# Performance work log

Measured on AMD Instinct MI355X. Metric: run time of the kernel, lower is better.

Reference implementation:

```python
import jax, jax.numpy as jnp
import numpy as np

B, S, D = 4, 4096, 1024
DFF = 4 * D
ACTIVE = 1024  # ceil(S * 0.25)


def setup_inputs() -> dict:
    key = jax.random.key(0)
    ks = jax.random.split(key, 4)
    x = jax.random.normal(ks[0], (B, S, D), dtype=jnp.float32)
    rw = jax.random.normal(ks[1], (D,), dtype=jnp.float32) * 0.02
    rb = jnp.zeros((1,), dtype=jnp.float32)
    w1 = jax.random.normal(ks[2], (D, DFF), dtype=jnp.float32) * 0.02
    b1 = jnp.zeros((DFF,), dtype=jnp.float32)
    w2 = jax.random.normal(ks[3], (DFF, D), dtype=jnp.float32) * 0.02
    b2 = jnp.zeros((D,), dtype=jnp.float32)
    return {"x": x, "rw": rw, "rb": rb, "w1": w1, "b1": b1,
            "w2": w2, "b2": b2, "active_tokens": ACTIVE}


def reference(x, rw, rb, w1, b1, w2, b2, active_tokens):
    b, s, d = x.shape
    # router: Linear(n_embd, 1) -> [B, S] scores
    scores = jnp.einsum('bsd,d->bs', x, rw) + rb[0]
    # top-k tokens per batch row
    _, idx = jax.lax.top_k(scores, active_tokens)          # [B, K] int32
    sel = jnp.take_along_axis(x, idx[..., None], axis=1)   # [B, K, D]
    # dense MLP on selected tokens (exact GELU as in torch nn.GELU)
    h = jax.nn.gelu(jnp.einsum('bkd,df->bkf', sel, w1) + b1, approximate=False)
    out = jnp.einsum('bkf,fd->bkd', h, w2) + b2            # [B, K, D]
    # sigmoid gate from router scores of selected tokens
    gates = jax.nn.sigmoid(jnp.take_along_axis(scores, idx, axis=1))  # [B, K]
    out = out * gates[..., None]
    # scatter back into zeros at selected positions
    flat_idx = (idx + jnp.arange(b, dtype=idx.dtype)[:, None] * s).reshape(-1)
    flat_out = jnp.zeros((b * s, d), dtype=out.dtype)
    flat_out = flat_out.at[flat_idx].set(out.reshape(-1, d))
    return flat_out.reshape(b, s, d)
```

## Files before the change

### kernel.cpp

```cpp
#include <hip/hip_runtime.h>
#include <hip/hip_bf16.h>
#include <cstdint>
#include <cstddef>

#define Bz 4
#define Sz 4096
#define Dz 1024
#define DFFz 4096
#define KACT 1024

typedef __bf16 bf16;
typedef __attribute__((ext_vector_type(8))) __bf16 bf16x8;
typedef __attribute__((ext_vector_type(4))) __bf16 bf16x4;
typedef __attribute__((ext_vector_type(4))) float f32x4;

__device__ __forceinline__ void async16(const void* g, void* l) {
  __builtin_amdgcn_global_load_lds(
      (const __attribute__((address_space(1))) void*)g,
      (__attribute__((address_space(3))) void*)l, 16, 0, 0);
}

__global__ __launch_bounds__(256) void prep_k(const float* __restrict__ x,
                                              const float* __restrict__ rw,
                                              const float* __restrict__ rb,
                                              float* __restrict__ scores,
                                              float4* __restrict__ out4,
                                              const float* __restrict__ w1,
                                              bf16* __restrict__ w1T,
                                              const float* __restrict__ w2,
                                              bf16* __restrict__ w2T) {
  __shared__ float t[32][33];
  const int bid = blockIdx.x;
  const int tid = threadIdx.x;
  if (bid < 4096) {
    int row = bid * 4 + (tid >> 6);
    int lane = tid & 63;
    const float4* xr = (const float4*)(x + (size_t)row * Dz);
    const float4* wr = (const float4*)rw;
    float acc = 0.f;
#pragma unroll
    for (int i = 0; i < 4; ++i) {
      float4 a = xr[lane + i * 64];
      float4 w = wr[lane + i * 64];
      acc += a.x * w.x + a.y * w.y + a.z * w.z + a.w * w.w;
    }
#pragma unroll
    for (int d = 32; d; d >>= 1) acc += __shfl_down(acc, d, 64);
    if (lane == 0) scores[row] = acc + rb[0];
    float4* o = out4 + (size_t)bid * 4 * (Dz / 4);
    const float4 z = make_float4(0.f, 0.f, 0.f, 0.f);
#pragma unroll
    for (int i = 0; i < 4; ++i) o[tid + i * 256] = z;
  } else {
    const float* in; bf16* outp; int R, C, bx, by;
    if (bid < 8192) {
      in = w1; outp = w1T; R = Dz; C = DFFz;
      bx = (bid - 4096) & 127; by = (bid - 4096) >> 7;
    } else {
      in = w2; outp = w2T; R = DFFz; C = Dz;
      bx = (bid - 8192) & 31; by = (bid - 8192) >> 5;
    }
    int c0 = bx * 32, r0 = by * 32;
    int tx = tid & 31, ty = tid >> 5;
#pragma unroll
    for (int i = 0; i < 32; i += 8) t[ty + i][tx] = in[(size_t)(r0 + ty + i) * C + c0 + tx];
    __syncthreads();
#pragma unroll
    for (int i = 0; i < 32; i += 8)
      outp[(size_t)(c0 + ty + i) * R + r0 + tx] = (bf16)t[tx][ty + i];
  }
}

__global__ __launch_bounds__(256) void select_gather_k(
    const float* __restrict__ x, const float* __restrict__ scores,
    int* __restrict__ sel_idx, float* __restrict__ gates, bf16* __restrict__ Xsel) {
  int b = blockIdx.x >> 8;
  int s0 = (blockIdx.x & 255) * 16;
  __shared__ float sc[Sz];
  __shared__ int red[16][4];
  __shared__ int rk[16];
  const int tid = threadIdx.x;
  const int wave = tid >> 6, lane = tid & 63;
  const float* srow = scores + (size_t)b * Sz;
#pragma unroll
  for (int i = 0; i < 4; ++i)
    ((float4*)sc)[tid + i * 256] = ((const float4*)srow)[tid + i * 256];
  __syncthreads();
  float mine[16];
#pragma unroll
  for (int j = 0; j < 16; ++j) mine[j] = sc[s0 + j];
  int cnt[16] = {};
  for (int t = tid; t < Sz; t += 256) {
    float o = sc[t];
#pragma unroll
    for (int j = 0; j < 16; ++j)
      cnt[j] += (o > mine[j]) || (o == mine[j] && t < s0 + j);
  }
#pragma unroll
  for (int j = 0; j < 16; ++j) {
    int c = cnt[j];
#pragma unroll
    for (int d = 32; d; d >>= 1) c += __shfl_down(c, d, 64);
    if (lane == 0) red[j][wave] = c;
  }
  __syncthreads();
  if (tid < 16) {
    int rank = red[tid][0] + red[tid][1] + red[tid][2] + red[tid][3];
    rk[tid] = rank;
    if (rank < KACT) {
      int m = b * KACT + rank;
      sel_idx[m] = s0 + tid;
      gates[m] = 1.f / (1.f + expf(-sc[s0 + tid]));
    }
  }
  __syncthreads();
#pragma unroll
  for (int j = 0; j < 16; ++j) {
    int rank = rk[j];
    if (rank >= KACT) continue;
    int m = b * KACT + rank;
    float4 v = ((const float4*)(x + ((size_t)b * Sz + s0 + j) * Dz))[tid];
    bf16x4 o = {(bf16)v.x, (bf16)v.y, (bf16)v.z, (bf16)v.w};
    ((bf16x4*)(Xsel + (size_t)m * Dz))[tid] = o;
  }
}

#define PROD_ISSUE(buf, k0)                                                    \
  async16(Ag + (k0), &As[buf][q * 8]);                                         \
  async16(Ag + (size_t)64 * K + (k0), &As[buf][2048 + q * 8]);                 \
  async16(Bg + (k0), &Bs[buf][q * 8]);                                         \
  async16(Bg + (size_t)64 * K + (k0), &Bs[buf][2048 + q * 8]);

#define PIPE_GEMM_BODY(KV, KOFF, NITER)                                        \
  __shared__ __align__(16) bf16 As[2][128 * 32];                 \
  __shared__ __align__(16) bf16 Bs[2][128 * 32];                               \
  constexpr int K = (KV);                                                      \
  const int tid = threadIdx.x;                                                 \
  const int wave = tid >> 6, lane = tid & 63;                                  \
  const int quad = lane >> 4, l16 = lane & 15;                                 \
  const int m0 = blockIdx.y * 128, n0 = blockIdx.x * 128;                      \
  const int wm = (wave >> 1) * 64, wn = (wave & 1) * 64;                       \
  const int q = tid & 255;                                                     \
  const bf16* Ag = A + (size_t)(m0 + (q >> 2)) * K + (KOFF) + (q & 3) * 8;     \
  const bf16* Bg = Bt + (size_t)(n0 + (q >> 2)) * K + (KOFF) + (q & 3) * 8;    \
  f32x4 acc[4][4] = {};                                                        \
  if (wave >= 4) { PROD_ISSUE(0, 0) }                                          \
  __syncthreads();                                                             \
  for (int it = 0; it < (NITER); ++it) {                                       \
    if (wave >= 4) {                                                           \
      if (it + 1 < (NITER)) { PROD_ISSUE((it + 1) & 1, (it + 1) * 32) }        \
    } else {                                                                   \
      const int cur = it & 1;                                                  \
      bf16x8 af[4], bfr[4];                                                    \
      _Pragma("unroll")                                                        \
      for (int i = 0; i < 4; ++i) {                                            \
        af[i] = *(const bf16x8*)&As[cur][(wm + i * 16 + l16) * 32 + quad * 8]; \
        bfr[i] = *(const bf16x8*)&Bs[cur][(wn + i * 16 + l16) * 32 + quad * 8]; \
      }                                                                        \
      _Pragma("unroll")                                                        \
      for (int mi = 0; mi < 4; ++mi)                                           \
        _Pragma("unroll")                                                      \
        for (int ni = 0; ni < 4; ++ni)                                         \
          acc[mi][ni] = __builtin_amdgcn_mfma_f32_16x16x32_bf16(af[mi], bfr[ni], acc[mi][ni], 0, 0, 0); \
    }                                                                          \
    __syncthreads();                                                           \
  }

__global__ __launch_bounds__(512, 4) void gemm1_k(const bf16* __restrict__ A,
                                                  const bf16* __restrict__ Bt,
                                                  const float* __restrict__ bias,
                                                  bf16* __restrict__ H) {
  constexpr int N = DFFz;
  PIPE_GEMM_BODY(Dz, 0, Dz / 32)
  if (wave < 4) {
#pragma unroll
    for (int mi = 0; mi < 4; ++mi) {
      int mbase = m0 + wm + mi * 16 + quad * 4;
#pragma unroll
      for (int ni = 0; ni < 4; ++ni) {
        int n = n0 + wn + ni * 16 + l16;
        float bn = bias[n];
#pragma unroll
        for (int r = 0; r < 4; ++r) {
          float z = acc[mi][ni][r] + bn;
          float g = 0.5f * z * (1.f + erff(z * 0.70710678118654752f));
          H[(size_t)(mbase + r) * N + n] = (bf16)g;
        }
      }
    }
  }
}

__global__ __launch_bounds__(512, 4) void gemm2_k(const bf16* __restrict__ A,
                                                  const bf16* __restrict__ Bt,
                                                  bf16* __restrict__ P) {
  PIPE_GEMM_BODY(DFFz, blockIdx.z * 2048, 2048 / 32)
  if (wave < 4) {
    bf16* Pc = P + (size_t)blockIdx.z * Bz * KACT * Dz;
#pragma unroll
    for (int mi = 0; mi < 4; ++mi) {
      int mbase = m0 + wm + mi * 16 + quad * 4;
#pragma unroll
      for (int ni = 0; ni < 4; ++ni) {
        int n = n0 + wn + ni * 16 + l16;
#pragma unroll
        for (int r = 0; r < 4; ++r)
          Pc[(size_t)(mbase + r) * Dz + n] = (bf16)acc[mi][ni][r];
      }
    }
  }
}

__global__ __launch_bounds__(256) void reduce_k(const bf16* __restrict__ P,
                                                const float* __restrict__ bias,
                                                const int* __restrict__ sel_idx,
                                                const float* __restrict__ gates,
                                                float* __restrict__ out) {
  int m = blockIdx.x;
  int b = m >> 10;
  int s = sel_idx[m];
  float gt = gates[m];
  int tid = threadIdx.x;
  const bf16x4* p0 = (const bf16x4*)(P + (size_t)m * Dz);
  const bf16x4* p1 = (const bf16x4*)(P + (size_t)Bz * KACT * Dz + (size_t)m * Dz);
  const float4* bv = (const float4*)bias;
  float4* orow = (float4*)(out + ((size_t)b * Sz + s) * Dz);
  bf16x4 a = p0[tid], c = p1[tid];
  float4 bb = bv[tid];
  float4 o;
  o.x = ((float)a[0] + (float)c[0] + bb.x) * gt;
  o.y = ((float)a[1] + (float)c[1] + bb.y) * gt;
  o.z = ((float)a[2] + (float)c[2] + bb.z) * gt;
  o.w = ((float)a[3] + (float)c[3] + bb.w) * gt;
  orow[tid] = o;
}

extern "C" void kernel_launch(void* const* d_in, const int* in_sizes, int n_in,
                              void* d_out, int out_size, void* d_ws, size_t ws_size,
                              hipStream_t stream) {
  (void)in_sizes; (void)n_in; (void)out_size; (void)ws_size;
  const float* x  = (const float*)d_in[0];
  const float* rw = (const float*)d_in[1];
  const float* rb = (const float*)d_in[2];
  const float* w1 = (const float*)d_in[3];
  const float* b1 = (const float*)d_in[4];
  const float* w2 = (const float*)d_in[5];
  const float* b2 = (const float*)d_in[6];
  float* out = (float*)d_out;

  char* ws = (char*)d_ws;
  float* scores = (float*)ws;  ws += (size_t)Bz * Sz * 4;
  int*   sel_idx = (int*)ws;   ws += (size_t)Bz * KACT * 4;
  float* gates = (float*)ws;   ws += (size_t)Bz * KACT * 4;
  bf16*  w2T = (bf16*)ws;      ws += (size_t)Dz * DFFz * 2;
  bf16*  H = (bf16*)ws;        ws += (size_t)Bz * KACT * DFFz * 2;
  bf16*  w1T = (bf16*)ws;      ws += (size_t)DFFz * Dz * 2;
  bf16*  Xsel = (bf16*)ws;     ws += (size_t)Bz * KACT * Dz * 2;
  bf16*  P = w1T;

  prep_k<<<3 * 4096, 256, 0, stream>>>(x, rw, rb, scores, (float4*)out, w1, w1T, w2, w2T);
  select_gather_k<<<Bz * (Sz / 16), 256, 0, stream>>>(x, scores, sel_idx, gates, Xsel);
  gemm1_k<<<dim3(DFFz / 128, (Bz * KACT) / 128), 512, 0, stream>>>(Xsel, w1T, b1, H);
  gemm2_k<<<dim3(Dz / 128, (Bz * KACT) / 128, 2), 512, 0, stream>>>(H, w2T, P);
  reduce_k<<<Bz * KACT, 256, 0, stream>>>(P, b2, sel_idx, gates, out);
}
```

Before: 291.0 us.

## Replace warp-specialized double-buffered GEMM with single-buffer 256-thread GEMM

Both GEMM kernels drop the producer/consumer warp specialization (4 loader waves plus 4 MFMA waves with double-buffered LDS). They now use 256-thread blocks where every wave both issues the async global-to-LDS loads and computes, on a single LDS buffer with barriers around each k-step. This halves LDS per block and removes the idle producer waves, which may allow more blocks per CU. The cost is that loads for the next k-tile no longer overlap compute within a block, so latency hiding depends on having other resident blocks.

```diff
diff --git a/kernel.cpp b/kernel.cpp
--- a/kernel.cpp
+++ b/kernel.cpp
@@ -125,88 +125,82 @@
   }
 }
 
-#define PROD_ISSUE(buf, k0)                                                    \
-  async16(Ag + (k0), &As[buf][q * 8]);                                         \
-  async16(Ag + (size_t)64 * K + (k0), &As[buf][2048 + q * 8]);                 \
-  async16(Bg + (k0), &Bs[buf][q * 8]);                                         \
-  async16(Bg + (size_t)64 * K + (k0), &Bs[buf][2048 + q * 8]);
-
-#define PIPE_GEMM_BODY(KV, KOFF, NITER)                                        \
-  __shared__ __align__(16) bf16 As[2][128 * 32];                 \
-  __shared__ __align__(16) bf16 Bs[2][128 * 32];                               \
+#define STAGE128(k0)                                                           \
+  {                                                                            \
+    async16(Ag + (k0), &As[tid * 8]);                                          \
+    async16(Ag + (size_t)64 * K + (k0), &As[2048 + tid * 8]);                  \
+    async16(Bg + (k0), &Bs[tid * 8]);                                          \
+    async16(Bg + (size_t)64 * K + (k0), &Bs[2048 + tid * 8]);                  \
+  }
+
+#define GEMM128_BODY(KV, KOFF, NITER)                                          \
+  __shared__ __align__(16) bf16 As[128 * 32];                        \
+  __shared__ __align__(16) bf16 Bs[128 * 32];                        \
   constexpr int K = (KV);                                                      \
   const int tid = threadIdx.x;                                                 \
   const int wave = tid >> 6, lane = tid & 63;                                  \
   const int quad = lane >> 4, l16 = lane & 15;                                 \
   const int m0 = blockIdx.y * 128, n0 = blockIdx.x * 128;                      \
   const int wm = (wave >> 1) * 64, wn = (wave & 1) * 64;                       \
-  const int q = tid & 255;                                                     \
-  const bf16* Ag = A + (size_t)(m0 + (q >> 2)) * K + (KOFF) + (q & 3) * 8;     \
-  const bf16* Bg = Bt + (size_t)(n0 + (q >> 2)) * K + (KOFF) + (q & 3) * 8;    \
+    \
+   \
+  const bf16* Ag = A + (size_t)(m0 + (tid >> 2)) * K + (KOFF) + (tid & 3) * 8; \
+  const bf16* Bg = Bt + (size_t)(n0 + (tid >> 2)) * K + (KOFF) + (tid & 3) * 8;\
   f32x4 acc[4][4] = {};                                                        \
-  if (wave >= 4) { PROD_ISSUE(0, 0) }                                          \
-  __syncthreads();                                                             \
+  STAGE128(0)                                                                  \
   for (int it = 0; it < (NITER); ++it) {                                       \
-    if (wave >= 4) {                                                           \
-      if (it + 1 < (NITER)) { PROD_ISSUE((it + 1) & 1, (it + 1) * 32) }        \
-    } else {                                                                   \
-      const int cur = it & 1;                                                  \
-      bf16x8 af[4], bfr[4];                                                    \
+    __syncthreads();                 \
+    bf16x8 af[4], bfr[4];                                                      \
+    _Pragma("unroll")                                                          \
+    for (int i = 0; i < 4; ++i) {                                              \
+      af[i] = *(const bf16x8*)&As[(wm + i * 16 + l16) * 32 + quad * 8];        \
+      bfr[i] = *(const bf16x8*)&Bs[(wn + i * 16 + l16) * 32 + quad * 8];       \
+    }                                                                          \
+    _Pragma("unroll")                                                          \
+    for (int mi = 0; mi < 4; ++mi)                                             \
       _Pragma("unroll")                                                        \
-      for (int i = 0; i < 4; ++i) {                                            \
-        af[i] = *(const bf16x8*)&As[cur][(wm + i * 16 + l16) * 32 + quad * 8]; \
-        bfr[i] = *(const bf16x8*)&Bs[cur][(wn + i * 16 + l16) * 32 + quad * 8]; \
-      }                                                                        \
-      _Pragma("unroll")                                                        \
-      for (int mi = 0; mi < 4; ++mi)                                           \
-        _Pragma("unroll")                                                      \
-        for (int ni = 0; ni < 4; ++ni)                                         \
-          acc[mi][ni] = __builtin_amdgcn_mfma_f32_16x16x32_bf16(af[mi], bfr[ni], acc[mi][ni], 0, 0, 0); \
-    }                                                                          \
-    __syncthreads();                                                           \
-  }
-
-__global__ __launch_bounds__(512, 4) void gemm1_k(const bf16* __restrict__ A,
-                                                  const bf16* __restrict__ Bt,
-                                                  const float* __restrict__ bias,
-                                                  bf16* __restrict__ H) {
-  constexpr int N = DFFz;
-  PIPE_GEMM_BODY(Dz, 0, Dz / 32)
-  if (wave < 4) {
-#pragma unroll
-    for (int mi = 0; mi < 4; ++mi) {
-      int mbase = m0 + wm + mi * 16 + quad * 4;
-#pragma unroll
-      for (int ni = 0; ni < 4; ++ni) {
-        int n = n0 + wn + ni * 16 + l16;
-        float bn = bias[n];
-#pragma unroll
-        for (int r = 0; r < 4; ++r) {
-          float z = acc[mi][ni][r] + bn;
-          float g = 0.5f * z * (1.f + erff(z * 0.70710678118654752f));
-          H[(size_t)(mbase + r) * N + n] = (bf16)g;
-        }
+      for (int ni = 0; ni < 4; ++ni)                                           \
+        acc[mi][ni] = __builtin_amdgcn_mfma_f32_16x16x32_bf16(af[mi], bfr[ni], acc[mi][ni], 0, 0, 0); \
+    __syncthreads();              \
+    if (it + 1 < (NITER)) { STAGE128((it + 1) * 32) }                          \
+  }
+
+__global__ __launch_bounds__(256) void gemm1_k(const bf16* __restrict__ A,
+                                               const bf16* __restrict__ Bt,
+                                               const float* __restrict__ bias,
+                                               bf16* __restrict__ H) {
+  GEMM128_BODY(Dz, 0, Dz / 32)
+#pragma unroll
+  for (int mi = 0; mi < 4; ++mi) {
+    int mbase = m0 + wm + mi * 16 + quad * 4;
+#pragma unroll
+    for (int ni = 0; ni < 4; ++ni) {
+      int n = n0 + wn + ni * 16 + l16;
+      float bn = bias[n];
+#pragma unroll
+      for (int r = 0; r < 4; ++r) {
+        float z = acc[mi][ni][r] + bn;
+        float g = 0.5f * z * (1.f + erff(z * 0.70710678118654752f));
+        H[(size_t)(mbase + r) * DFFz + n] = (bf16)g;
       }
     }
   }
 }
 
-__global__ __launch_bounds__(512, 4) void gemm2_k(const bf16* __restrict__ A,
-                                                  const bf16* __restrict__ Bt,
-                                                  bf16* __restrict__ P) {
-  PIPE_GEMM_BODY(DFFz, blockIdx.z * 2048, 2048 / 32)
-  if (wave < 4) {
-    bf16* Pc = P + (size_t)blockIdx.z * Bz * KACT * Dz;
-#pragma unroll
-    for (int mi = 0; mi < 4; ++mi) {
-      int mbase = m0 + wm + mi * 16 + quad * 4;
-#pragma unroll
-      for (int ni = 0; ni < 4; ++ni) {
-        int n = n0 + wn + ni * 16 + l16;
-#pragma unroll
-        for (int r = 0; r < 4; ++r)
-          Pc[(size_t)(mbase + r) * Dz + n] = (bf16)acc[mi][ni][r];
-      }
+__global__ __launch_bounds__(256) void gemm2_k(const bf16* __restrict__ A,
+                                               const bf16* __restrict__ Bt,
+                                               bf16* __restrict__ P) {
+  GEMM128_BODY(DFFz, blockIdx.z * 2048, 2048 / 32)
+  bf16* Pc = P + (size_t)blockIdx.z * Bz * KACT * Dz;
+#pragma unroll
+  for (int mi = 0; mi < 4; ++mi) {
+    int mbase = m0 + wm + mi * 16 + quad * 4;
+#pragma unroll
+    for (int ni = 0; ni < 4; ++ni) {
+      int n = n0 + wn + ni * 16 + l16;
+#pragma unroll
+      for (int r = 0; r < 4; ++r)
+        Pc[(size_t)(mbase + r) * Dz + n] = (bf16)acc[mi][ni][r];
     }
   }
 }
@@ -260,7 +254,7 @@
 
   prep_k<<<3 * 4096, 256, 0, stream>>>(x, rw, rb, scores, (float4*)out, w1, w1T, w2, w2T);
   select_gather_k<<<Bz * (Sz / 16), 256, 0, stream>>>(x, scores, sel_idx, gates, Xsel);
-  gemm1_k<<<dim3(DFFz / 128, (Bz * KACT) / 128), 512, 0, stream>>>(Xsel, w1T, b1, H);
-  gemm2_k<<<dim3(Dz / 128, (Bz * KACT) / 128, 2), 512, 0, stream>>>(H, w2T, P);
+  gemm1_k<<<dim3(DFFz / 128, (Bz * KACT) / 128), 256, 0, stream>>>(Xsel, w1T, b1, H);
+  gemm2_k<<<dim3(Dz / 128, (Bz * KACT) / 128, 2), 256, 0, stream>>>(H, w2T, P);
   reduce_k<<<Bz * KACT, 256, 0, stream>>>(P, b2, sel_idx, gates, out);
 }
```

New measurement: 300.9 us. 1.03x slower.
